# Performance work log

Measured on AMD Instinct MI355X. Metric: run time of the kernel, lower is better.

The kernel has to match this reference:

```python
import jax, jax.numpy as jnp
import numpy as np

K_LAYERS = 10
ALPHA = 0.1
N_NODES = 100_000
N_EDGES = 1_600_000
D_FEAT = 64


def setup_inputs() -> dict:
    key = jax.random.key(0)
    k1, k2, k3 = jax.random.split(key, 3)
    features = jax.random.normal(k1, (N_NODES, D_FEAT), dtype=jnp.float32)
    src = jax.random.randint(k2, (N_EDGES,), 0, N_NODES, dtype=jnp.int64)
    dst = jax.random.randint(k3, (N_EDGES,), 0, N_NODES, dtype=jnp.int64)
    return {"features": features, "src": src, "dst": dst}


def reference(features, src, dst):
    # APPNP forward (eval mode: feature dropout and edge_drop are identity).
    n = features.shape[0]
    ones = jnp.ones((src.shape[0],), dtype=features.dtype)
    deg_out = jax.ops.segment_sum(ones, src, num_segments=n)
    deg_in = jax.ops.segment_sum(ones, dst, num_segments=n)
    norm_src = jnp.clip(deg_out, 1.0) ** -0.5  # [N]
    norm_dst = jnp.clip(deg_in, 1.0) ** -0.5   # [N]

    h0 = features
    h = features
    for _ in range(K_LAYERS):
        # D_out^{-1/2} scaling, gather to edges, scatter-sum to dst, D_in^{-1/2}
        msg = (h * norm_src[:, None])[src]               # [E, d]
        agg = jax.ops.segment_sum(msg, dst, num_segments=n)  # [N, d]
        h = (1.0 - ALPHA) * (agg * norm_dst[:, None]) + ALPHA * h0
    return h
```

## Files before the change

### kernel.cpp

```cpp
#include <hip/hip_runtime.h>
#include <hip/hip_fp16.h>
#include <stdint.h>

#define D_FEAT 64
#define K_LAYERS 10
#define SCAN_CHUNK 2048

__global__ void deg_kernel(const int* __restrict__ src, const int* __restrict__ dst,
                           int* deg_out, int* deg_in, int E) {
    int i = blockIdx.x * blockDim.x + threadIdx.x;
    int base = i * 4;
    if (base + 3 < E) {
        int4 s4 = *(const int4*)(src + base);
        int4 d4 = *(const int4*)(dst + base);
        atomicAdd(&deg_out[s4.x], 1); atomicAdd(&deg_in[d4.x], 1);
        atomicAdd(&deg_out[s4.y], 1); atomicAdd(&deg_in[d4.y], 1);
        atomicAdd(&deg_out[s4.z], 1); atomicAdd(&deg_in[d4.z], 1);
        atomicAdd(&deg_out[s4.w], 1); atomicAdd(&deg_in[d4.w], 1);
    } else {
        for (int j = base; j < E; ++j) {
            atomicAdd(&deg_out[src[j]], 1);
            atomicAdd(&deg_in[dst[j]], 1);
        }
    }
}

__global__ void norm_kernel(const int* __restrict__ deg_out, const int* __restrict__ deg_in,
                            float* __restrict__ ns, float* __restrict__ nd, int N) {
    int i = blockIdx.x * blockDim.x + threadIdx.x;
    if (i < N) {
        ns[i] = rsqrtf(fmaxf((float)deg_out[i], 1.0f));
        nd[i] = rsqrtf(fmaxf((float)deg_in[i], 1.0f));
    }
}

__global__ void cvt_kernel(const float* __restrict__ in, __half* __restrict__ out, int n8) {
    int i = blockIdx.x * blockDim.x + threadIdx.x;
    if (i < n8) {
        float4 a = *((const float4*)in + 2 * i);
        float4 b = *((const float4*)in + 2 * i + 1);
        __half2 o[4];
        o[0] = __float22half2_rn(make_float2(a.x, a.y));
        o[1] = __float22half2_rn(make_float2(a.z, a.w));
        o[2] = __float22half2_rn(make_float2(b.x, b.y));
        o[3] = __float22half2_rn(make_float2(b.z, b.w));
        *((float4*)out + i) = *(const float4*)o;
    }
}

__global__ void chunk_sum_kernel(const int* __restrict__ deg, int N, int* __restrict__ partials) {
    __shared__ int sdata[256];
    constexpr int PT = SCAN_CHUNK / 256;
    int base = blockIdx.x * SCAN_CHUNK;
    int t = threadIdx.x;
    int s = 0;
#pragma unroll
    for (int j = 0; j < PT; ++j) {
        int idx = base + t * PT + j;
        if (idx < N) s += deg[idx];
    }
    sdata[t] = s;
    __syncthreads();
    for (int off = 128; off > 0; off >>= 1) {
        if (t < off) sdata[t] += sdata[t + off];
        __syncthreads();
    }
    if (t == 0) partials[blockIdx.x] = sdata[0];
}

__global__ void scan_partials_kernel(int* partials, int nchunks, int* row_ptr, int N, int E) {
    if (threadIdx.x == 0 && blockIdx.x == 0) {
        int s = 0;
        for (int i = 0; i < nchunks; ++i) { int v = partials[i]; partials[i] = s; s += v; }
        row_ptr[N] = E;
    }
}

__global__ void chunk_scan_kernel(const int* __restrict__ deg, int N,
                                  const int* __restrict__ partials, int* __restrict__ row_ptr) {
    __shared__ int sdata[256];
    constexpr int PT = SCAN_CHUNK / 256;
    int base = blockIdx.x * SCAN_CHUNK;
    int t = threadIdx.x;
    int vals[PT];
    int s = 0;
#pragma unroll
    for (int j = 0; j < PT; ++j) {
        int idx = base + t * PT + j;
        int v = (idx < N) ? deg[idx] : 0;
        vals[j] = s;
        s += v;
    }
    sdata[t] = s;
    __syncthreads();
    for (int off = 1; off < 256; off <<= 1) {
        int v = (t >= off) ? sdata[t - off] : 0;
        __syncthreads();
        sdata[t] += v;
        __syncthreads();
    }
    int texcl = (t > 0) ? sdata[t - 1] : 0;
    int off0 = partials[blockIdx.x];
#pragma unroll
    for (int j = 0; j < PT; ++j) {
        int idx = base + t * PT + j;
        if (idx < N) row_ptr[idx] = off0 + texcl + vals[j];
    }
}

__global__ void fill_kernel(const int* __restrict__ src, const int* __restrict__ dst,
                            const float* __restrict__ ns, const float* __restrict__ nd,
                            int* cursor, uint2* __restrict__ edges, int E) {
    int i = blockIdx.x * blockDim.x + threadIdx.x;
    int base = i * 4;
    if (base + 3 < E) {
        int4 s4 = *(const int4*)(src + base);
        int4 d4 = *(const int4*)(dst + base);
#pragma unroll
        for (int j = 0; j < 4; ++j) {
            int s = (j == 0) ? s4.x : (j == 1) ? s4.y : (j == 2) ? s4.z : s4.w;
            int d = (j == 0) ? d4.x : (j == 1) ? d4.y : (j == 2) ? d4.z : d4.w;
            int pos = atomicAdd(&cursor[d], 1);
            float w = ns[s] * nd[d];
            edges[pos] = make_uint2((unsigned)s, __float_as_uint(w));
        }
    } else {
        for (int j = base; j < E; ++j) {
            int d = dst[j];
            int s = src[j];
            int pos = atomicAdd(&cursor[d], 1);
            float w = ns[s] * nd[d];
            edges[pos] = make_uint2((unsigned)s, __float_as_uint(w));
        }
    }
}

template <bool LAST>
__global__ __launch_bounds__(256) void prop_kernel(
    const __half* __restrict__ h, const __half* __restrict__ h0,
    const uint2* __restrict__ edges, const int* __restrict__ row_ptr,
    void* __restrict__ out, int N)
{
    int gid  = blockIdx.x * blockDim.x + threadIdx.x;
    int node = gid >> 6;
    if (node >= N) return;
    int lane = threadIdx.x & 63;
    int grp  = lane >> 3;
    int fl   = lane & 7;

    int start = row_ptr[node];
    int end   = row_ptr[node + 1];

    float acc[8];
#pragma unroll
    for (int j = 0; j < 8; ++j) acc[j] = 0.f;

    auto do_edge = [&](int e) {
        uint2 r = edges[e];
        float4 raw = *((const float4*)(h + ((size_t)r.x << 6)) + fl);
        float w = __uint_as_float(r.y);
        const __half2* hp = (const __half2*)&raw;
#pragma unroll
        for (int k = 0; k < 4; ++k) {
            float2 f = __half22float2(hp[k]);
            acc[2 * k]     = fmaf(w, f.x, acc[2 * k]);
            acc[2 * k + 1] = fmaf(w, f.y, acc[2 * k + 1]);
        }
    };

    int e = start + grp;
    for (; e + 8 < end; e += 16) {
        uint2 r0 = edges[e];
        uint2 r1 = edges[e + 8];
        float4 v0 = *((const float4*)(h + ((size_t)r0.x << 6)) + fl);
        float4 v1 = *((const float4*)(h + ((size_t)r1.x << 6)) + fl);
        float w0 = __uint_as_float(r0.y);
        float w1 = __uint_as_float(r1.y);
        const __half2* p0 = (const __half2*)&v0;
        const __half2* p1 = (const __half2*)&v1;
#pragma unroll
        for (int k = 0; k < 4; ++k) {
            float2 f0 = __half22float2(p0[k]);
            float2 f1 = __half22float2(p1[k]);
            acc[2 * k]     = fmaf(w0, f0.x, acc[2 * k]);
            acc[2 * k + 1] = fmaf(w0, f0.y, acc[2 * k + 1]);
            acc[2 * k]     = fmaf(w1, f1.x, acc[2 * k]);
            acc[2 * k + 1] = fmaf(w1, f1.y, acc[2 * k + 1]);
        }
    }
    if (e < end) do_edge(e);

#pragma unroll
    for (int j = 0; j < 8; ++j) acc[j] += __shfl_xor(acc[j], 8, 64);
#pragma unroll
    for (int j = 0; j < 8; ++j) acc[j] += __shfl_xor(acc[j], 16, 64);
#pragma unroll
    for (int j = 0; j < 8; ++j) acc[j] += __shfl_xor(acc[j], 32, 64);

    if (grp == 0) {
        float4 braw = *((const float4*)(h0 + ((size_t)node << 6)) + fl);
        const __half2* bp = (const __half2*)&braw;
        float r[8];
#pragma unroll
        for (int k = 0; k < 4; ++k) {
            float2 f = __half22float2(bp[k]);
            r[2 * k]     = fmaf(0.9f, acc[2 * k],     0.1f * f.x);
            r[2 * k + 1] = fmaf(0.9f, acc[2 * k + 1], 0.1f * f.y);
        }
        if (!LAST) {
            __half2 o[4];
#pragma unroll
            for (int k = 0; k < 4; ++k)
                o[k] = __float22half2_rn(make_float2(r[2 * k], r[2 * k + 1]));
            *((float4*)((__half*)out + ((size_t)node << 6)) + fl) = *(const float4*)o;
        } else {
            float4* op = (float4*)((float*)out + ((size_t)node << 6));
            op[2 * fl]     = make_float4(r[0], r[1], r[2], r[3]);
            op[2 * fl + 1] = make_float4(r[4], r[5], r[6], r[7]);
        }
    }
}

extern "C" void kernel_launch(void* const* d_in, const int* in_sizes, int n_in,
                              void* d_out, int out_size, void* d_ws, size_t ws_size,
                              hipStream_t stream) {
    const float* features = (const float*)d_in[0];
    const int*   src      = (const int*)d_in[1];
    const int*   dst      = (const int*)d_in[2];
    const int E = in_sizes[1];
    const int N = in_sizes[0] / D_FEAT;

    char* ws = (char*)d_ws;
    size_t off = 0;
    auto alloc = [&](size_t bytes, size_t align) -> char* {
        off = (off + align - 1) & ~(align - 1);
        char* p = ws + off;
        off += bytes;
        return p;
    };
    int*    deg_out = (int*)alloc(4 * (size_t)N, 4);
    int*    deg_in  = (int*)alloc(4 * (size_t)N, 4);
    int*    cursor  = (int*)alloc(4 * (size_t)N, 4);
    int*    row_ptr = (int*)alloc(4 * ((size_t)N + 1), 4);
    float*  ns      = (float*)alloc(4 * (size_t)N, 4);
    float*  nd      = (float*)alloc(4 * (size_t)N, 4);
    int nchunks = (N + SCAN_CHUNK - 1) / SCAN_CHUNK;
    int*    partials = (int*)alloc(4 * (size_t)nchunks, 4);
    uint2*  edges   = (uint2*)alloc(8 * (size_t)E, 16);
    __half* feat16  = (__half*)alloc(2 * (size_t)N * D_FEAT, 16);
    __half* hbufA   = (__half*)alloc(2 * (size_t)N * D_FEAT, 16);
    __half* hbufB   = (__half*)alloc(2 * (size_t)N * D_FEAT, 16);

    hipMemsetAsync(deg_out, 0, 4 * (size_t)N * 2, stream);

    int ethreads4 = (E + 3) / 4;
    deg_kernel<<<(ethreads4 + 255) / 256, 256, 0, stream>>>(src, dst, deg_out, deg_in, E);

    int n8 = N * D_FEAT / 8;
    cvt_kernel<<<(n8 + 255) / 256, 256, 0, stream>>>(features, feat16, n8);

    norm_kernel<<<(N + 255) / 256, 256, 0, stream>>>(deg_out, deg_in, ns, nd, N);
    chunk_sum_kernel<<<nchunks, 256, 0, stream>>>(deg_in, N, partials);
    scan_partials_kernel<<<1, 64, 0, stream>>>(partials, nchunks, row_ptr, N, E);
    chunk_scan_kernel<<<nchunks, 256, 0, stream>>>(deg_in, N, partials, row_ptr);
    hipMemcpyAsync(cursor, row_ptr, 4 * (size_t)N, hipMemcpyDeviceToDevice, stream);
    fill_kernel<<<(ethreads4 + 255) / 256, 256, 0, stream>>>(src, dst, ns, nd, cursor, edges, E);

    const __half* h_in = feat16;
    int prop_blocks = (int)(((size_t)N * 64 + 255) / 256);
    for (int k = 0; k < K_LAYERS - 1; ++k) {
        __half* h_out = (k & 1) ? hbufB : hbufA;
        prop_kernel<false><<<prop_blocks, 256, 0, stream>>>(h_in, feat16, edges, row_ptr, h_out, N);
        h_in = h_out;
    }
    prop_kernel<true><<<prop_blocks, 256, 0, stream>>>(h_in, feat16, edges, row_ptr, d_out, N);
}
```

Measured before the change: 759.1 us.

## Fold edge weights into pre-scaled node features and drop per-edge weight storage

The propagation is rewritten in terms of g = D_out^{-1/2} h, so each layer sums raw neighbour rows and applies a per-node scale, 0.9*ns*nd, once at the end. The per-edge weight array goes away and the CSR stores only 4-byte source indices, which halves edge traffic in each of the ten layers. CSR fill now uses ranks taken from the degree atomics instead of a second atomic cursor pass, and the feature conversion is merged into the fill kernel. Intermediate layers store the scaled features and the scaled residual in fp16, which shifts where rounding happens.

After: 728.8 us. 1.04x faster.

```diff
diff --git a/kernel.cpp b/kernel.cpp
--- a/kernel.cpp
+++ b/kernel.cpp
@@ -7,44 +7,40 @@
 #define SCAN_CHUNK 2048
 
 __global__ void deg_kernel(const int* __restrict__ src, const int* __restrict__ dst,
-                           int* deg_out, int* deg_in, int E) {
+                           int* deg_out, int* deg_in, int* __restrict__ rank, int E) {
     int i = blockIdx.x * blockDim.x + threadIdx.x;
     int base = i * 4;
     if (base + 3 < E) {
         int4 s4 = *(const int4*)(src + base);
         int4 d4 = *(const int4*)(dst + base);
-        atomicAdd(&deg_out[s4.x], 1); atomicAdd(&deg_in[d4.x], 1);
-        atomicAdd(&deg_out[s4.y], 1); atomicAdd(&deg_in[d4.y], 1);
-        atomicAdd(&deg_out[s4.z], 1); atomicAdd(&deg_in[d4.z], 1);
-        atomicAdd(&deg_out[s4.w], 1); atomicAdd(&deg_in[d4.w], 1);
+        atomicAdd(&deg_out[s4.x], 1);
+        atomicAdd(&deg_out[s4.y], 1);
+        atomicAdd(&deg_out[s4.z], 1);
+        atomicAdd(&deg_out[s4.w], 1);
+        int4 r;
+        r.x = atomicAdd(&deg_in[d4.x], 1);
+        r.y = atomicAdd(&deg_in[d4.y], 1);
+        r.z = atomicAdd(&deg_in[d4.z], 1);
+        r.w = atomicAdd(&deg_in[d4.w], 1);
+        *(int4*)(rank + base) = r;
     } else {
         for (int j = base; j < E; ++j) {
             atomicAdd(&deg_out[src[j]], 1);
-            atomicAdd(&deg_in[dst[j]], 1);
+            rank[j] = atomicAdd(&deg_in[dst[j]], 1);
         }
     }
 }
 
 __global__ void norm_kernel(const int* __restrict__ deg_out, const int* __restrict__ deg_in,
-                            float* __restrict__ ns, float* __restrict__ nd, int N) {
+                            float* __restrict__ ns, float* __restrict__ nd,
+                            float* __restrict__ cvec, int N) {
     int i = blockIdx.x * blockDim.x + threadIdx.x;
     if (i < N) {
-        ns[i] = rsqrtf(fmaxf((float)deg_out[i], 1.0f));
-        nd[i] = rsqrtf(fmaxf((float)deg_in[i], 1.0f));
-    }
-}
-
-__global__ void cvt_kernel(const float* __restrict__ in, __half* __restrict__ out, int n8) {
-    int i = blockIdx.x * blockDim.x + threadIdx.x;
-    if (i < n8) {
-        float4 a = *((const float4*)in + 2 * i);
-        float4 b = *((const float4*)in + 2 * i + 1);
-        __half2 o[4];
-        o[0] = __float22half2_rn(make_float2(a.x, a.y));
-        o[1] = __float22half2_rn(make_float2(a.z, a.w));
-        o[2] = __float22half2_rn(make_float2(b.x, b.y));
-        o[3] = __float22half2_rn(make_float2(b.z, b.w));
-        *((float4*)out + i) = *(const float4*)o;
+        float a = rsqrtf(fmaxf((float)deg_out[i], 1.0f));
+        float b = rsqrtf(fmaxf((float)deg_in[i], 1.0f));
+        ns[i] = a;
+        nd[i] = b;
+        cvec[i] = 0.9f * a * b;
     }
 }
 
@@ -108,37 +104,56 @@
     }
 }
 
-__global__ void fill_kernel(const int* __restrict__ src, const int* __restrict__ dst,
-                            const float* __restrict__ ns, const float* __restrict__ nd,
-                            int* cursor, uint2* __restrict__ edges, int E) {
-    int i = blockIdx.x * blockDim.x + threadIdx.x;
-    int base = i * 4;
-    if (base + 3 < E) {
-        int4 s4 = *(const int4*)(src + base);
-        int4 d4 = *(const int4*)(dst + base);
-#pragma unroll
-        for (int j = 0; j < 4; ++j) {
-            int s = (j == 0) ? s4.x : (j == 1) ? s4.y : (j == 2) ? s4.z : s4.w;
-            int d = (j == 0) ? d4.x : (j == 1) ? d4.y : (j == 2) ? d4.z : d4.w;
-            int pos = atomicAdd(&cursor[d], 1);
-            float w = ns[s] * nd[d];
-            edges[pos] = make_uint2((unsigned)s, __float_as_uint(w));
+__global__ void fill_cvt_kernel(const int* __restrict__ src, const int* __restrict__ dst,
+                                const int* __restrict__ rank, const int* __restrict__ row_ptr,
+                                unsigned* __restrict__ edge_src, int E, int fillBlocks,
+                                const float* __restrict__ features, const float* __restrict__ ns,
+                                __half* __restrict__ g0, __half* __restrict__ f0g, int N) {
+    int b = blockIdx.x;
+    if (b < fillBlocks) {
+        int i = b * blockDim.x + threadIdx.x;
+        int base = i * 4;
+        if (base + 3 < E) {
+            int4 s4 = *(const int4*)(src + base);
+            int4 d4 = *(const int4*)(dst + base);
+            int4 r4 = *(const int4*)(rank + base);
+            edge_src[row_ptr[d4.x] + r4.x] = (unsigned)s4.x;
+            edge_src[row_ptr[d4.y] + r4.y] = (unsigned)s4.y;
+            edge_src[row_ptr[d4.z] + r4.z] = (unsigned)s4.z;
+            edge_src[row_ptr[d4.w] + r4.w] = (unsigned)s4.w;
+        } else {
+            for (int j = base; j < E; ++j)
+                edge_src[row_ptr[dst[j]] + rank[j]] = (unsigned)src[j];
         }
     } else {
-        for (int j = base; j < E; ++j) {
-            int d = dst[j];
-            int s = src[j];
-            int pos = atomicAdd(&cursor[d], 1);
-            float w = ns[s] * nd[d];
-            edges[pos] = make_uint2((unsigned)s, __float_as_uint(w));
+        int t = (b - fillBlocks) * blockDim.x + threadIdx.x;
+        if (t < N * (D_FEAT / 8)) {
+            int node = t >> 3;
+            float s = ns[node];
+            float4 a = *((const float4*)features + 2 * t);
+            float4 c = *((const float4*)features + 2 * t + 1);
+            __half2 og[4], of[4];
+        og[0] = __float22half2_rn(make_float2(s * a.x, s * a.y));
+        og[1] = __float22half2_rn(make_float2(s * a.z, s * a.w));
+        og[2] = __float22half2_rn(make_float2(s * c.x, s * c.y));
+        og[3] = __float22half2_rn(make_float2(s * c.z, s * c.w));
+        float sf = 0.1f * s;
+        of[0] = __float22half2_rn(make_float2(sf * a.x, sf * a.y));
+        of[1] = __float22half2_rn(make_float2(sf * a.z, sf * a.w));
+        of[2] = __float22half2_rn(make_float2(sf * c.x, sf * c.y));
+        of[3] = __float22half2_rn(make_float2(sf * c.z, sf * c.w));
+            *((float4*)g0 + t)  = *(const float4*)og;
+            *((float4*)f0g + t) = *(const float4*)of;
         }
     }
 }
 
 template <bool LAST>
 __global__ __launch_bounds__(256) void prop_kernel(
-    const __half* __restrict__ h, const __half* __restrict__ h0,
-    const uint2* __restrict__ edges, const int* __restrict__ row_ptr,
+    const __half* __restrict__ g, const __half* __restrict__ f0g,
+    const float* __restrict__ features,
+    const unsigned* __restrict__ edge_src, const int* __restrict__ row_ptr,
+    const float* __restrict__ cvec, const float* __restrict__ nd,
     void* __restrict__ out, int N)
 {
     int gid  = blockIdx.x * blockDim.x + threadIdx.x;
@@ -155,40 +170,33 @@
 #pragma unroll
     for (int j = 0; j < 8; ++j) acc[j] = 0.f;
 
-    auto do_edge = [&](int e) {
-        uint2 r = edges[e];
-        float4 raw = *((const float4*)(h + ((size_t)r.x << 6)) + fl);
-        float w = __uint_as_float(r.y);
-        const __half2* hp = (const __half2*)&raw;
-#pragma unroll
-        for (int k = 0; k < 4; ++k) {
-            float2 f = __half22float2(hp[k]);
-            acc[2 * k]     = fmaf(w, f.x, acc[2 * k]);
-            acc[2 * k + 1] = fmaf(w, f.y, acc[2 * k + 1]);
-        }
-    };
-
     int e = start + grp;
     for (; e + 8 < end; e += 16) {
-        uint2 r0 = edges[e];
-        uint2 r1 = edges[e + 8];
-        float4 v0 = *((const float4*)(h + ((size_t)r0.x << 6)) + fl);
-        float4 v1 = *((const float4*)(h + ((size_t)r1.x << 6)) + fl);
-        float w0 = __uint_as_float(r0.y);
-        float w1 = __uint_as_float(r1.y);
+        unsigned s0 = edge_src[e];
+        unsigned s1 = edge_src[e + 8];
+        float4 v0 = *((const float4*)(g + ((size_t)s0 << 6)) + fl);
+        float4 v1 = *((const float4*)(g + ((size_t)s1 << 6)) + fl);
         const __half2* p0 = (const __half2*)&v0;
         const __half2* p1 = (const __half2*)&v1;
 #pragma unroll
         for (int k = 0; k < 4; ++k) {
             float2 f0 = __half22float2(p0[k]);
             float2 f1 = __half22float2(p1[k]);
-            acc[2 * k]     = fmaf(w0, f0.x, acc[2 * k]);
-            acc[2 * k + 1] = fmaf(w0, f0.y, acc[2 * k + 1]);
-            acc[2 * k]     = fmaf(w1, f1.x, acc[2 * k]);
-            acc[2 * k + 1] = fmaf(w1, f1.y, acc[2 * k + 1]);
-        }
-    }
-    if (e < end) do_edge(e);
+            acc[2 * k]     += f0.x + f1.x;
+            acc[2 * k + 1] += f0.y + f1.y;
+        }
+    }
+    if (e < end) {
+        unsigned s0 = edge_src[e];
+        float4 v0 = *((const float4*)(g + ((size_t)s0 << 6)) + fl);
+        const __half2* p0 = (const __half2*)&v0;
+#pragma unroll
+        for (int k = 0; k < 4; ++k) {
+            float2 f0 = __half22float2(p0[k]);
+            acc[2 * k]     += f0.x;
+            acc[2 * k + 1] += f0.y;
+        }
+    }
 
 #pragma unroll
     for (int j = 0; j < 8; ++j) acc[j] += __shfl_xor(acc[j], 8, 64);
@@ -198,25 +206,35 @@
     for (int j = 0; j < 8; ++j) acc[j] += __shfl_xor(acc[j], 32, 64);
 
     if (grp == 0) {
-        float4 braw = *((const float4*)(h0 + ((size_t)node << 6)) + fl);
-        const __half2* bp = (const __half2*)&braw;
-        float r[8];
-#pragma unroll
-        for (int k = 0; k < 4; ++k) {
-            float2 f = __half22float2(bp[k]);
-            r[2 * k]     = fmaf(0.9f, acc[2 * k],     0.1f * f.x);
-            r[2 * k + 1] = fmaf(0.9f, acc[2 * k + 1], 0.1f * f.y);
-        }
         if (!LAST) {
+            float cm = cvec[node];
+            float4 braw = *((const float4*)(f0g + ((size_t)node << 6)) + fl);
+            const __half2* bp = (const __half2*)&braw;
             __half2 o[4];
 #pragma unroll
-            for (int k = 0; k < 4; ++k)
-                o[k] = __float22half2_rn(make_float2(r[2 * k], r[2 * k + 1]));
+            for (int k = 0; k < 4; ++k) {
+                float2 f = __half22float2(bp[k]);
+                o[k] = __float22half2_rn(make_float2(fmaf(cm, acc[2 * k], f.x),
+                                                     fmaf(cm, acc[2 * k + 1], f.y)));
+            }
             *((float4*)((__half*)out + ((size_t)node << 6)) + fl) = *(const float4*)o;
         } else {
+            float w = 0.9f * nd[node];
+            const float4* fp = (const float4*)(features + ((size_t)node << 6));
+            float4 b0 = fp[2 * fl];
+            float4 b1 = fp[2 * fl + 1];
+            float4 o0, o1;
+            o0.x = fmaf(w, acc[0], 0.1f * b0.x);
+            o0.y = fmaf(w, acc[1], 0.1f * b0.y);
+            o0.z = fmaf(w, acc[2], 0.1f * b0.z);
+            o0.w = fmaf(w, acc[3], 0.1f * b0.w);
+            o1.x = fmaf(w, acc[4], 0.1f * b1.x);
+            o1.y = fmaf(w, acc[5], 0.1f * b1.y);
+            o1.z = fmaf(w, acc[6], 0.1f * b1.z);
+            o1.w = fmaf(w, acc[7], 0.1f * b1.w);
             float4* op = (float4*)((float*)out + ((size_t)node << 6));
-            op[2 * fl]     = make_float4(r[0], r[1], r[2], r[3]);
-            op[2 * fl + 1] = make_float4(r[4], r[5], r[6], r[7]);
+            op[2 * fl]     = o0;
+            op[2 * fl + 1] = o1;
         }
     }
 }
@@ -238,40 +256,43 @@
         off += bytes;
         return p;
     };
-    int*    deg_out = (int*)alloc(4 * (size_t)N, 4);
-    int*    deg_in  = (int*)alloc(4 * (size_t)N, 4);
-    int*    cursor  = (int*)alloc(4 * (size_t)N, 4);
-    int*    row_ptr = (int*)alloc(4 * ((size_t)N + 1), 4);
-    float*  ns      = (float*)alloc(4 * (size_t)N, 4);
-    float*  nd      = (float*)alloc(4 * (size_t)N, 4);
+    int*      deg_out  = (int*)alloc(4 * (size_t)N, 4);
+    int*      deg_in   = (int*)alloc(4 * (size_t)N, 4);
+    int*      row_ptr  = (int*)alloc(4 * ((size_t)N + 1), 4);
+    float*    ns       = (float*)alloc(4 * (size_t)N, 4);
+    float*    nd       = (float*)alloc(4 * (size_t)N, 4);
+    float*    cvec     = (float*)alloc(4 * (size_t)N, 4);
     int nchunks = (N + SCAN_CHUNK - 1) / SCAN_CHUNK;
-    int*    partials = (int*)alloc(4 * (size_t)nchunks, 4);
-    uint2*  edges   = (uint2*)alloc(8 * (size_t)E, 16);
-    __half* feat16  = (__half*)alloc(2 * (size_t)N * D_FEAT, 16);
-    __half* hbufA   = (__half*)alloc(2 * (size_t)N * D_FEAT, 16);
-    __half* hbufB   = (__half*)alloc(2 * (size_t)N * D_FEAT, 16);
+    int*      partials = (int*)alloc(4 * (size_t)nchunks, 4);
+    int*      rank     = (int*)alloc(4 * (size_t)E, 16);
+    unsigned* edge_src = (unsigned*)alloc(4 * (size_t)E, 16);
+    __half*   f0g      = (__half*)alloc(2 * (size_t)N * D_FEAT, 16);
+    __half*   gA       = (__half*)alloc(2 * (size_t)N * D_FEAT, 16);
+    __half*   gB       = (__half*)alloc(2 * (size_t)N * D_FEAT, 16);
 
     hipMemsetAsync(deg_out, 0, 4 * (size_t)N * 2, stream);
 
     int ethreads4 = (E + 3) / 4;
-    deg_kernel<<<(ethreads4 + 255) / 256, 256, 0, stream>>>(src, dst, deg_out, deg_in, E);
-
-    int n8 = N * D_FEAT / 8;
-    cvt_kernel<<<(n8 + 255) / 256, 256, 0, stream>>>(features, feat16, n8);
-
-    norm_kernel<<<(N + 255) / 256, 256, 0, stream>>>(deg_out, deg_in, ns, nd, N);
+    int eblocks = (ethreads4 + 255) / 256;
+    deg_kernel<<<eblocks, 256, 0, stream>>>(src, dst, deg_out, deg_in, rank, E);
+    norm_kernel<<<(N + 255) / 256, 256, 0, stream>>>(deg_out, deg_in, ns, nd, cvec, N);
     chunk_sum_kernel<<<nchunks, 256, 0, stream>>>(deg_in, N, partials);
     scan_partials_kernel<<<1, 64, 0, stream>>>(partials, nchunks, row_ptr, N, E);
     chunk_scan_kernel<<<nchunks, 256, 0, stream>>>(deg_in, N, partials, row_ptr);
-    hipMemcpyAsync(cursor, row_ptr, 4 * (size_t)N, hipMemcpyDeviceToDevice, stream);
-    fill_kernel<<<(ethreads4 + 255) / 256, 256, 0, stream>>>(src, dst, ns, nd, cursor, edges, E);
-
-    const __half* h_in = feat16;
+
+    int cvtThreads = N * (D_FEAT / 8);
+    int cvtBlocks = (cvtThreads + 255) / 256;
+    fill_cvt_kernel<<<eblocks + cvtBlocks, 256, 0, stream>>>(
+        src, dst, rank, row_ptr, edge_src, E, eblocks, features, ns, gA, f0g, N);
+
     int prop_blocks = (int)(((size_t)N * 64 + 255) / 256);
+    const __half* h_in = gA;
     for (int k = 0; k < K_LAYERS - 1; ++k) {
-        __half* h_out = (k & 1) ? hbufB : hbufA;
-        prop_kernel<false><<<prop_blocks, 256, 0, stream>>>(h_in, feat16, edges, row_ptr, h_out, N);
+        __half* h_out = (k & 1) ? gA : gB;
+        prop_kernel<false><<<prop_blocks, 256, 0, stream>>>(
+            h_in, f0g, features, edge_src, row_ptr, cvec, nd, h_out, N);
         h_in = h_out;
     }
-    prop_kernel<true><<<prop_blocks, 256, 0, stream>>>(h_in, feat16, edges, row_ptr, d_out, N);
-}
+    prop_kernel<true><<<prop_blocks, 256, 0, stream>>>(
+        h_in, f0g, features, edge_src, row_ptr, cvec, nd, d_out, N);
+}
```
